# Kernel tuning notes

Measured on AMD Instinct MI355X. Metric: run time of the kernel, lower is better.

## Reference

```python
import jax, jax.numpy as jnp
import numpy as np

STEPS_PER_DAY = 144
HEADS = 4
MODEL_D = 152  # 24 input + 24 tod + 24 dow + 80 adaptive
HEAD_D = MODEL_D // HEADS
FF_D = 256
L = 12
PRED = 12
N = 358
B = 16
EVT_D = 1024
HID_EVT = 256
NUM_EVT = 4096
KMAX = 8
NEG = -1e30


def _layer_norm(x, g, b, eps=1e-5):
    m = jnp.mean(x, -1, keepdims=True)
    v = jnp.mean((x - m) ** 2, -1, keepdims=True)
    return (x - m) * jax.lax.rsqrt(v + eps) * g + b


def _mha(x, Wq, bq, Wk, bk, Wv, bv, Wo, bo):
    # x: (B, A, S, D); self-attention over axis S
    b_, a_, s_, d_ = x.shape
    q = (x @ Wq + bq).reshape(b_, a_, s_, HEADS, HEAD_D)
    k = (x @ Wk + bk).reshape(b_, a_, s_, HEADS, HEAD_D)
    v = (x @ Wv + bv).reshape(b_, a_, s_, HEADS, HEAD_D)
    scores = jnp.einsum('baqhd,bakhd->bahqk', q, k) * (HEAD_D ** -0.5)
    attn = jax.nn.softmax(scores, axis=-1)
    out = jnp.einsum('bahqk,bakhd->baqhd', attn, v).reshape(b_, a_, s_, d_)
    return out @ Wo + bo


def setup_inputs() -> dict:
    key = jax.random.key(0)
    ks = jax.random.split(key, 24)
    f32 = jnp.float32

    def nrm(k, shape, s=0.02):
        return jax.random.normal(k, shape, dtype=f32) * s

    inp = {}
    inp['var_x'] = jax.random.normal(ks[0], (B, L, N, 1), dtype=f32)
    inp['marker_x'] = jax.random.uniform(ks[1], (B, L, N, 4), dtype=f32)
    inp['W_in'] = nrm(ks[2], (3, 24)); inp['b_in'] = jnp.zeros((24,), f32)
    inp['tod_emb'] = nrm(ks[3], (STEPS_PER_DAY, 24))
    inp['dow_emb'] = nrm(ks[4], (7, 24))
    inp['adaptive_emb'] = nrm(ks[5], (L, N, 80))
    inp['Wq'] = nrm(ks[6], (6, MODEL_D, MODEL_D)); inp['bq'] = jnp.zeros((6, MODEL_D), f32)
    inp['Wk'] = nrm(ks[7], (6, MODEL_D, MODEL_D)); inp['bk'] = jnp.zeros((6, MODEL_D), f32)
    inp['Wv'] = nrm(ks[8], (6, MODEL_D, MODEL_D)); inp['bv'] = jnp.zeros((6, MODEL_D), f32)
    inp['Wo'] = nrm(ks[9], (6, MODEL_D, MODEL_D)); inp['bo'] = jnp.zeros((6, MODEL_D), f32)
    inp['W1'] = nrm(ks[10], (6, MODEL_D, FF_D)); inp['b1'] = jnp.zeros((6, FF_D), f32)
    inp['W2'] = nrm(ks[11], (6, FF_D, MODEL_D)); inp['b2'] = jnp.zeros((6, MODEL_D), f32)
    inp['ln1_g'] = jnp.ones((6, MODEL_D), f32); inp['ln1_b'] = jnp.zeros((6, MODEL_D), f32)
    inp['ln2_g'] = jnp.ones((6, MODEL_D), f32); inp['ln2_b'] = jnp.zeros((6, MODEL_D), f32)
    inp['event_embeddings'] = nrm(ks[12], (NUM_EVT + 1, EVT_D)).at[0].set(0.0)
    inp['W_evt'] = nrm(ks[13], (EVT_D, HID_EVT)); inp['b_evt'] = jnp.zeros((HID_EVT,), f32)
    inp['W_mm'] = nrm(ks[14], (L * (MODEL_D + HID_EVT), PRED)); inp['b_mm'] = jnp.zeros((PRED,), f32)
    inp['W_ts'] = nrm(ks[15], (L * MODEL_D, PRED)); inp['b_ts'] = jnp.zeros((PRED,), f32)
    inp['doy_indices'] = jax.random.randint(ks[16], (366, KMAX), 1, NUM_EVT + 1, dtype=jnp.int32)
    mask = jax.random.uniform(ks[17], (366, KMAX)) < 0.6
    inp['doy_mask'] = mask.at[:, 0].set(True)
    return inp


def reference(var_x, marker_x, W_in, b_in, tod_emb, dow_emb, adaptive_emb,
              Wq, bq, Wk, bk, Wv, bv, Wo, bo, W1, b1, W2, b2,
              ln1_g, ln1_b, ln2_g, ln2_b, event_embeddings, W_evt, b_evt,
              W_mm, b_mm, W_ts, b_ts, doy_indices, doy_mask):
    b_, l_, n_, _ = var_x.shape
    tod = jnp.clip((marker_x[..., 0] * STEPS_PER_DAY).astype(jnp.int32), 0, STEPS_PER_DAY - 1)
    dow = jnp.clip((marker_x[..., 1] * 7).astype(jnp.int32), 0, 6)
    x_in = jnp.concatenate([var_x, marker_x[..., 0:1], marker_x[..., 1:2]], axis=-1)
    x = jnp.concatenate([
        x_in @ W_in + b_in,
        tod_emb[tod],
        dow_emb[dow],
        jnp.broadcast_to(adaptive_emb[None], (b_, l_, n_, adaptive_emb.shape[-1])),
    ], axis=-1)  # (B, L, N, MODEL_D)
    # 3 temporal attention layers (over L), then 3 spatial (over N)
    for i in range(6):
        temporal = i < 3
        h = jnp.swapaxes(x, 1, 2) if temporal else x
        out = _mha(h, Wq[i], bq[i], Wk[i], bk[i], Wv[i], bv[i], Wo[i], bo[i])
        h = _layer_norm(h + out, ln1_g[i], ln1_b[i])
        ff = jax.nn.relu(h @ W1[i] + b1[i]) @ W2[i] + b2[i]
        h = _layer_norm(h + ff, ln2_g[i], ln2_b[i])
        x = jnp.swapaxes(h, 1, 2) if temporal else h
    ts_emb = jnp.swapaxes(x, 1, 2)  # (B, N, L, D)
    # ragged event gather + linear + masked max-pool (one vectorized pass)
    doy = jnp.clip((marker_x[:, -1, 0, 3] * 365).astype(jnp.int32), 0, 365)
    idx = doy_indices[doy]           # (B, KMAX)
    msk = doy_mask[doy]              # (B, KMAX)
    h_evt = event_embeddings[idx] @ W_evt + b_evt  # (B, KMAX, HID_EVT)
    evt = jnp.max(jnp.where(msk[..., None], h_evt, NEG), axis=1)  # (B, HID_EVT)
    evt_b = jnp.broadcast_to(evt[:, None, None, :], (b_, n_, l_, HID_EVT))
    fused = jnp.concatenate([evt_b, ts_emb], axis=-1).reshape(b_, n_, -1)
    mm_pred = fused @ W_mm + b_mm
    ts_pred = ts_emb.reshape(b_, n_, -1) @ W_ts + b_ts
    return jnp.swapaxes(mm_pred + ts_pred, 1, 2)  # (B, PRED, N)
```

## Files before the change

kernel.cpp:

```cpp
#include <hip/hip_runtime.h>
#include <hip/hip_bf16.h>

using bf = __hip_bfloat16;

#define B_   16
#define L_   12
#define N_   358
#define D_   152
#define TOK_ (B_*L_*N_)
#define FF_  256
#define HD_  38
#define SCALE_ 0.16222142113076254f
#define C2_   0.23403921469340696f

__device__ __forceinline__ float bf2f(bf x) { return __bfloat162float(x); }
__device__ __forceinline__ bf f2bf(float f) { return __float2bfloat16(f); }
__device__ __forceinline__ float lo_bf(unsigned u) { return __uint_as_float(u << 16); }
__device__ __forceinline__ float hi_bf(unsigned u) { return __uint_as_float(u & 0xffff0000u); }
__device__ __forceinline__ unsigned pk_bf(float a, float b) {
  union { bf h; unsigned short u; } A, Bu;
  A.h = f2bf(a); Bu.h = f2bf(b);
  return ((unsigned)Bu.u << 16) | A.u;
}
__device__ __forceinline__ ushort f2bf_u(float f) {
  union { bf h; ushort u; } t; t.h = f2bf(f); return t.u;
}

using short8  = __attribute__((ext_vector_type(8))) short;
using float4v = __attribute__((ext_vector_type(4))) float;

__device__ __forceinline__ void gl_lds16(const void* g, void* l) {
  __builtin_amdgcn_global_load_lds(
      (const __attribute__((address_space(1))) void*)g,
      (__attribute__((address_space(3))) void*)l, 16, 0, 0);
}

template<int SUBCB>
__device__ __forceinline__ void issue_w8(const char* gsrc, ushort* lds, int w, int lane) {
  constexpr int TB = SUBCB >> 10;
  constexpr int TAIL = SUBCB & 1023;
#pragma unroll
  for (int blk0 = 0; blk0 < TB; blk0 += 8) {
    int blk = blk0 + w;
    if (blk < TB)
      gl_lds16(gsrc + blk*1024 + (size_t)lane*16, (char*)lds + blk*1024);
  }
  if (TAIL) {
    if (w == (TB & 7) && lane < TAIL/16)
      gl_lds16(gsrc + TB*1024 + (size_t)lane*16, (char*)lds + TB*1024);
  }
}

template<int SUBCB>
__device__ __forceinline__ int issue_cnt(int w) {
  constexpr int TB = SUBCB >> 10;
  constexpr int TAIL = SUBCB & 1023;
  int n = (TB > 8 && w < TB - 8) ? 2 : 1;
  if (TAIL && w == (TB & 7)) n += 1;
  return n;
}

__device__ __forceinline__ void vm_wait(int n) {
  if (n == 1)      asm volatile("s_waitcnt vmcnt(1)" ::: "memory");
  else if (n == 2) asm volatile("s_waitcnt vmcnt(2)" ::: "memory");
  else             asm volatile("s_waitcnt vmcnt(3)" ::: "memory");
}

__device__ __forceinline__ short8 ld_g8(const ushort* p) {
  union { unsigned u[4]; short8 v; } t;
  t.u[0] = *(const unsigned*)(p);
  t.u[1] = *(const unsigned*)(p + 2);
  t.u[2] = *(const unsigned*)(p + 4);
  t.u[3] = *(const unsigned*)(p + 6);
  return t.v;
}

__global__ void k_beacon(float* out, int n, float val) {
  int i = blockIdx.x * 256 + threadIdx.x;
  if (i < n) out[i] = val;
}

#define WPREP_B 2700
#define EMB_B   269
#define EVT_B   128
#define WC_B    86
#define PREP_B  (WPREP_B + EMB_B + EVT_B + WC_B)

__device__ void d_wprep(int bid, int tid,
    const float* __restrict__ Wq, const float* __restrict__ Wk,
    const float* __restrict__ Wv, const float* __restrict__ Wo,
    const float* __restrict__ W1, const float* __restrict__ W2,
    unsigned* __restrict__ out) {
  int i = bid * 256 + tid;
  if (i >= 6*115200) return;
  int layer = i / 115200, r = i % 115200;
  const float* src; int K, Nd, d, up, c;
  if (r < 48000) {
    c = r / 9600; int rr = r % 9600; int m = rr / 3200; int r2 = rr % 3200;
    d = r2 / 20; up = r2 % 20;
    src = (m == 0 ? Wq : (m == 1 ? Wk : Wv)) + layer*23104; K = 152; Nd = 152;
  } else if (r < 64000) {
    int rr = r - 48000; c = rr / 3200; int r2 = rr % 3200;
    d = r2 / 20; up = r2 % 20;
    src = Wo + layer*23104; K = 152; Nd = 152;
  } else if (r < 89600) {
    int rr = r - 64000; c = rr / 5120; int r2 = rr % 5120;
    d = r2 / 20; up = r2 % 20;
    src = W1 + layer*38912; K = 152; Nd = 256;
  } else {
    int rr = r - 89600; c = rr / 3200; int r2 = rr % 3200;
    d = r2 / 20; up = r2 % 20;
    src = W2 + layer*38912; K = 256; Nd = 152;
  }
  float v0 = 0.f, v1 = 0.f;
  int k0 = 32*c + 2*up;
  if (up < 16 && d < Nd) {
    if (k0 < K)     v0 = src[(long)k0*Nd + d];
    if (k0 + 1 < K) v1 = src[(long)(k0+1)*Nd + d];
  }
  out[i] = pk_bf(v0, v1);
}

__device__ void d_embed(int bid, int tid,
    const float* __restrict__ var_x, const float* __restrict__ marker,
    const float* __restrict__ W_in, const float* __restrict__ b_in,
    const float* __restrict__ tod_emb, const float* __restrict__ dow_emb,
    const float* __restrict__ adap, bf* __restrict__ x) {
  int t = bid * 256 + tid;
  if (t >= TOK_) return;
  int n = t % N_;
  int l = (t / N_) % L_;
  float var = var_x[t];
  float m0 = marker[t*4 + 0];
  float m1 = marker[t*4 + 1];
  int tod = (int)(m0 * 144.f); tod = tod < 0 ? 0 : (tod > 143 ? 143 : tod);
  int dw  = (int)(m1 * 7.f);   dw  = dw  < 0 ? 0 : (dw  > 6   ? 6   : dw);
  bf* xp = x + (long)t * D_;
  for (int d = 0; d < 24; ++d)
    xp[d] = f2bf(var * W_in[d] + m0 * W_in[24 + d] + m1 * W_in[48 + d] + b_in[d]);
  for (int d = 0; d < 24; ++d) xp[24 + d] = f2bf(tod_emb[tod*24 + d]);
  for (int d = 0; d < 24; ++d) xp[48 + d] = f2bf(dow_emb[dw*24 + d]);
  for (int d = 0; d < 80; ++d) xp[72 + d] = f2bf(adap[(l*N_ + n)*80 + d]);
}

__device__ void d_evt1(int bk, int tid,
    const float* __restrict__ marker, const int* __restrict__ doy_idx,
    const float* __restrict__ emb, const float* __restrict__ W_evt,
    const float* __restrict__ b_evt, float* __restrict__ evt_h) {
  int b = bk >> 3; int ks = bk & 7;
  float m3 = marker[((b*L_ + (L_-1))*N_ + 0)*4 + 3];
  int doy = (int)(m3 * 365.f); doy = doy < 0 ? 0 : (doy > 365 ? 365 : doy);
  int idx = doy_idx[doy*8 + ks];
  if (idx < 0 || idx > 4096) idx = 0;
  int d = tid;
  float acc = b_evt[d];
  const float* er = emb + (long)idx * 1024;
  for (int e = 0; e < 1024; ++e)
    acc += er[e] * W_evt[e*256 + d];
  evt_h[bk*256 + d] = acc;
}

__device__ void d_wcomb(int bid, int tid,
    const float* __restrict__ W_mm, const float* __restrict__ W_ts,
    float* __restrict__ wcomb, float* __restrict__ wevtsum) {
  int i = bid * 256 + tid;
  if (i < 1824*12) {
    int r = i / 12, p = i % 12, l = r / 152, d = r % 152;
    wcomb[i] = W_mm[(l*408 + 256 + d)*12 + p] + W_ts[i];
  }
  if (i < 256*12) {
    int e = i / 12, p = i % 12;
    float s = 0.f;
    for (int l = 0; l < 12; ++l) s += W_mm[(l*408 + e)*12 + p];
    wevtsum[i] = s;
  }
}

__global__ __launch_bounds__(256) void k_prep(
    const float* Wq, const float* Wk, const float* Wv, const float* Wo,
    const float* W1, const float* W2, unsigned* wout,
    const float* var_x, const float* marker, const float* W_in,
    const float* b_in, const float* tod_emb, const float* dow_emb,
    const float* adap, bf* x,
    const int* doyi, const float* emb, const float* W_evt,
    const float* b_evt, float* evt_h,
    const float* W_mm, const float* W_ts, float* wcomb, float* wevtsum) {
  int bid = blockIdx.x, tid = threadIdx.x;
  if (bid < WPREP_B)
    d_wprep(bid, tid, Wq, Wk, Wv, Wo, W1, W2, wout);
  else if (bid < WPREP_B + EMB_B)
    d_embed(bid - WPREP_B, tid, var_x, marker, W_in, b_in, tod_emb, dow_emb, adap, x);
  else if (bid < WPREP_B + EMB_B + EVT_B)
    d_evt1(bid - WPREP_B - EMB_B, tid, marker, doyi, emb, W_evt, b_evt, evt_h);
  else
    d_wcomb(bid - WPREP_B - EMB_B - EVT_B, tid, W_mm, W_ts, wcomb, wevtsum);
}

template<int K, int Nd, int NW, int TOKB, int CSPLIT, bool RELU, bool LN>
__global__ __launch_bounds__(512) void k_gemm7(
    const bf* __restrict__ X, const ushort* __restrict__ Wg,
    const float* __restrict__ bi0, const float* __restrict__ bi1,
    const float* __restrict__ bi2, const bf* __restrict__ Res,
    const float* __restrict__ g, const float* __restrict__ bb,
    bf* __restrict__ Y0, bf* __restrict__ Y1, bf* __restrict__ Y2) {
  constexpr int NJ   = (Nd + 15) / 16;
  constexpr int NdP  = NJ * 16;
  constexpr int KC   = (K + 31) / 32;
  constexpr int G    = NW * CSPLIT;
  constexpr int S    = KC * G;
  constexpr int IR   = NdP / CSPLIT;
  constexpr int SUB_USH = IR * 40;
  constexpr int SUBCB   = SUB_USH * 2;
  constexpr int NJW  = IR / 32;
  constexpr int MR   = TOKB / 64;
  constexpr bool GLX = (K == 152);
  constexpr int XSTR = GLX ? K : (K + 8);
  __shared__ __align__(16) ushort Xs[TOKB * XSTR + 8];
  __shared__ __align__(16) ushort Wb[2 * SUB_USH];
  long row0 = (long)blockIdx.x * TOKB;
  int tid = threadIdx.x;
  int lane = tid & 63, w = tid >> 6;
  int cl = lane & 15, gr = lane >> 4;
  int wr = w >> 1, wc = w & 1;
  if constexpr (GLX) {
    constexpr int TBX = TOKB * K * 2 / 1024;
    const char* Xgc = (const char*)(X + row0 * K);
#pragma unroll
    for (int b0 = 0; b0 < TBX; b0 += 8) {
      int blk = b0 + w;
      if (blk < TBX)
        gl_lds16(Xgc + blk*1024 + (size_t)lane*16, (char*)Xs + blk*1024);
    }
  } else {
    const char* Xgc = (const char*)(X + row0 * K);
    for (int i = tid; i < TOKB*(K/8); i += 512) {
      int r = i / (K/8), c = i % (K/8);
      *(short8*)&Xs[r*XSTR + 8*c] = *(const short8*)(Xgc + r*(K*2) + c*16);
    }
    __syncthreads();
  }
  const char* gW = (const char*)Wg;
  issue_w8<SUBCB>(gW, Wb, w, lane);
  const int nw = issue_cnt<SUBCB>(w);
  float4v acc[G][MR][NJW];
#pragma unroll
  for (int gi = 0; gi < G; ++gi)
#pragma unroll
    for (int mi = 0; mi < MR; ++mi)
#pragma unroll
      for (int j = 0; j < NJW; ++j) acc[gi][mi][j] = (float4v){0.f,0.f,0.f,0.f};
#pragma unroll
  for (int s = 0; s < S; ++s) {
    if (s + 1 < S) {
      issue_w8<SUBCB>(gW + (size_t)(s+1)*SUBCB, Wb + ((s+1)&1)*SUB_USH, w, lane);
      vm_wait(nw);
    } else {
      asm volatile("s_waitcnt vmcnt(0)" ::: "memory");
    }
    __builtin_amdgcn_s_barrier();
    int kc = (s / G) * 32;
    const ushort* wb = Wb + (s&1)*SUB_USH;
    short8 af[MR];
#pragma unroll
    for (int mi = 0; mi < MR; ++mi)
      af[mi] = *(const short8*)&Xs[((TOKB/4)*wr + 16*mi + cl)*XSTR + kc + 8*gr];
#pragma unroll
    for (int j = 0; j < NJW; ++j) {
      short8 bv = *(const short8*)&wb[((IR/2)*wc + 16*j + cl)*40 + 8*gr];
#pragma unroll
      for (int mi = 0; mi < MR; ++mi)
        acc[s % G][mi][j] =
            __builtin_amdgcn_mfma_f32_16x16x32_bf16(af[mi], bv, acc[s % G][mi][j], 0, 0, 0);
    }
    asm volatile("s_waitcnt lgkmcnt(0)" ::: "memory");
    __builtin_amdgcn_s_barrier();
  }
  if constexpr (!LN) {
#pragma unroll
    for (int gi = 0; gi < G; ++gi) {
      bf* Y = (NW > 1) ? (gi == 0 ? Y0 : (gi == 1 ? Y1 : Y2)) : Y0;
      const float* bp = (NW > 1) ? (gi == 0 ? bi0 : (gi == 1 ? bi1 : bi2)) : bi0;
      int colb = (CSPLIT > 1 ? IR*gi : 0) + (IR/2)*wc;
#pragma unroll
      for (int j = 0; j < NJW; ++j) {
        int col = colb + 16*j + cl;
        if (col < Nd) {
          float bvs = bp[col];
#pragma unroll
          for (int mi = 0; mi < MR; ++mi) {
            long rw = row0 + (TOKB/4)*wr + 16*mi + 4*gr;
#pragma unroll
            for (int r = 0; r < 4; ++r) {
              float val = acc[gi][mi][j][r] + bvs;
              if (RELU) val = fmaxf(val, 0.f);
              Y[(rw + r) * Nd + col] = f2bf(val);
            }
          }
        }
      }
    }
  } else {
    float* LNb = (float*)Wb;
    int colb = (IR/2)*wc;
#pragma unroll
    for (int j = 0; j < NJW; ++j) {
      int col = colb + 16*j + cl;
      if (col < Nd) {
        float bvs = bi0[col];
#pragma unroll
        for (int mi = 0; mi < MR; ++mi) {
          long rw = row0 + (TOKB/4)*wr + 16*mi + 4*gr;
#pragma unroll
          for (int r = 0; r < 4; ++r)
            acc[0][mi][j][r] += bvs + bf2f(Res[(rw + r) * Nd + col]);
        }
      }
    }
    float mean[MR][4], rs[MR][4];
#pragma unroll
    for (int mi = 0; mi < MR; ++mi)
#pragma unroll
      for (int r = 0; r < 4; ++r) {
        float s = 0.f;
#pragma unroll
        for (int j = 0; j < NJW; ++j) s += acc[0][mi][j][r];
        s += __shfl_xor(s, 1, 64); s += __shfl_xor(s, 2, 64);
        s += __shfl_xor(s, 4, 64); s += __shfl_xor(s, 8, 64);
        if (cl == 0) LNb[((wr*MR + mi)*2 + wc)*16 + 4*gr + r] = s;
      }
    __syncthreads();
#pragma unroll
    for (int mi = 0; mi < MR; ++mi)
#pragma unroll
      for (int r = 0; r < 4; ++r) {
        float tot = LNb[((wr*MR + mi)*2 + 0)*16 + 4*gr + r]
                  + LNb[((wr*MR + mi)*2 + 1)*16 + 4*gr + r];
        mean[mi][r] = tot * (1.f / (float)Nd);
      }
#pragma unroll
    for (int mi = 0; mi < MR; ++mi)
#pragma unroll
      for (int r = 0; r < 4; ++r) {
        float s2 = 0.f;
#pragma unroll
        for (int j = 0; j < NJW; ++j) {
          int col = colb + 16*j + cl;
          if (col < Nd) {
            float dv = acc[0][mi][j][r] - mean[mi][r];
            s2 += dv*dv;
          }
        }
        s2 += __shfl_xor(s2, 1, 64); s2 += __shfl_xor(s2, 2, 64);
        s2 += __shfl_xor(s2, 4, 64); s2 += __shfl_xor(s2, 8, 64);
        if (cl == 0) LNb[256 + ((wr*MR + mi)*2 + wc)*16 + 4*gr + r] = s2;
      }
    __syncthreads();
#pragma unroll
    for (int mi = 0; mi < MR; ++mi)
#pragma unroll
      for (int r = 0; r < 4; ++r) {
        float tot2 = LNb[256 + ((wr*MR + mi)*2 + 0)*16 + 4*gr + r]
                   + LNb[256 + ((wr*MR + mi)*2 + 1)*16 + 4*gr + r];
        rs[mi][r] = rsqrtf(tot2 * (1.f / (float)Nd) + 1e-5f);
      }
#pragma unroll
    for (int j = 0; j < NJW; ++j) {
      int col = colb + 16*j + cl;
      if (col < Nd) {
        float gv = g[col], bv2 = bb[col];
#pragma unroll
        for (int mi = 0; mi < MR; ++mi) {
          long rw = row0 + (TOKB/4)*wr + 16*mi + 4*gr;
#pragma unroll
          for (int r = 0; r < 4; ++r)
            Y0[(rw + r) * Nd + col] =
                f2bf((acc[0][mi][j][r] - mean[mi][r]) * rs[mi][r] * gv + bv2);
        }
      }
    }
  }
}

__global__ __launch_bounds__(512) void k_ffn(
    const bf* __restrict__ X, const ushort* __restrict__ W1g,
    const ushort* __restrict__ W2g,
    const float* __restrict__ b1, const float* __restrict__ b2,
    const bf* __restrict__ Res, const float* __restrict__ g,
    const float* __restrict__ bb, bf* __restrict__ Y) {
  constexpr int S1 = 10, SUB1 = 5120;
  constexpr int S2 = 8,  SUB2 = 6400;
  constexpr int HSTR = 260;
  __shared__ __align__(16) ushort S_[29440];
  ushort* Xs  = S_;
  ushort* W1b = S_ + 9728;
  ushort* Hs  = S_;
  ushort* W2b = S_ + 16640;
  long row0 = (long)blockIdx.x * 64;
  int tid = threadIdx.x, lane = tid & 63, w = tid >> 6;
  int cl = lane & 15, gr = lane >> 4;
  int wr = w >> 1, wc = w & 1;
  {
    const char* Xgc = (const char*)(X + row0 * 152);
#pragma unroll
    for (int b0 = 0; b0 < 19; b0 += 8) {
      int blk = b0 + w;
      if (blk < 19)
        gl_lds16(Xgc + blk*1024 + (size_t)lane*16, (char*)Xs + blk*1024);
    }
  }
  issue_w8<SUB1*2>((const char*)W1g, W1b, w, lane);
  const int nw1 = issue_cnt<SUB1*2>(w);
  const int nw2 = issue_cnt<SUB2*2>(w);
  float4v acc1[2][4];
#pragma unroll
  for (int g2 = 0; g2 < 2; ++g2)
#pragma unroll
    for (int j = 0; j < 4; ++j) acc1[g2][j] = (float4v){0.f,0.f,0.f,0.f};
#pragma unroll
  for (int s = 0; s < S1; ++s) {
    if (s + 1 < S1) {
      issue_w8<SUB1*2>((const char*)W1g + (size_t)(s+1)*SUB1*2,
                       W1b + ((s+1)&1)*SUB1, w, lane);
      vm_wait(nw1);
    } else {
      asm volatile("s_waitcnt vmcnt(0)" ::: "memory");
    }
    __builtin_amdgcn_s_barrier();
    int kc = (s / 2) * 32;
    const ushort* wb = W1b + (s&1)*SUB1;
    short8 af = *(const short8*)&Xs[(16*wr + cl)*152 + kc + 8*gr];
#pragma unroll
    for (int j = 0; j < 4; ++j) {
      short8 bv = *(const short8*)&wb[(64*wc + 16*j + cl)*40 + 8*gr];
      acc1[s&1][j] =
          __builtin_amdgcn_mfma_f32_16x16x32_bf16(af, bv, acc1[s&1][j], 0, 0, 0);
    }
    asm volatile("s_waitcnt lgkmcnt(0)" ::: "memory");
    __builtin_amdgcn_s_barrier();
  }
#pragma unroll
  for (int g2 = 0; g2 < 2; ++g2)
#pragma unroll
    for (int j = 0; j < 4; ++j) {
      int col = g2*128 + 64*wc + 16*j + cl;
      float bvs = b1[col];
#pragma unroll
      for (int r = 0; r < 4; ++r) {
        int row = 16*wr + 4*gr + r;
        Hs[row*HSTR + col] = f2bf_u(fmaxf(acc1[g2][j][r] + bvs, 0.f));
      }
    }
  issue_w8<SUB2*2>((const char*)W2g, W2b, w, lane);
  asm volatile("s_waitcnt lgkmcnt(0)" ::: "memory");
  __builtin_amdgcn_s_barrier();
  float4v acc2[5];
#pragma unroll
  for (int j = 0; j < 5; ++j) acc2[j] = (float4v){0.f,0.f,0.f,0.f};
#pragma unroll
  for (int s = 0; s < S2; ++s) {
    if (s + 1 < S2) {
      issue_w8<SUB2*2>((const char*)W2g + (size_t)(s+1)*SUB2*2,
                       W2b + ((s+1)&1)*SUB2, w, lane);
      vm_wait(nw2);
    } else {
      asm volatile("s_waitcnt vmcnt(0)" ::: "memory");
    }
    __builtin_amdgcn_s_barrier();
    int kc = s * 32;
    const ushort* wb = W2b + (s&1)*SUB2;
    short8 af = *(const short8*)&Hs[(16*wr + cl)*HSTR + kc + 8*gr];
#pragma unroll
    for (int j = 0; j < 5; ++j) {
      short8 bv = *(const short8*)&wb[(80*wc + 16*j + cl)*40 + 8*gr];
      acc2[j] =
          __builtin_amdgcn_mfma_f32_16x16x32_bf16(af, bv, acc2[j], 0, 0, 0);
    }
    asm volatile("s_waitcnt lgkmcnt(0)" ::: "memory");
    __builtin_amdgcn_s_barrier();
  }
  float* LNb = (float*)W2b;
  int colb = 80*wc;
#pragma unroll
  for (int j = 0; j < 5; ++j) {
    int col = colb + 16*j + cl;
    if (col < D_) {
      float bvs = b2[col];
#pragma unroll
      for (int r = 0; r < 4; ++r)
        acc2[j][r] += bvs + bf2f(Res[(row0 + 16*wr + 4*gr + r) * D_ + col]);
    }
  }
  float mean[4], rsv[4];
#pragma unroll
  for (int r = 0; r < 4; ++r) {
    float s = 0.f;
#pragma unroll
    for (int j = 0; j < 5; ++j)
      if (colb + 16*j + cl < D_) s += acc2[j][r];
    s += __shfl_xor(s, 1, 64); s += __shfl_xor(s, 2, 64);
    s += __shfl_xor(s, 4, 64); s += __shfl_xor(s, 8, 64);
    if (cl == 0) LNb[(wr*2 + wc)*16 + 4*gr + r] = s;
  }
  __syncthreads();
#pragma unroll
  for (int r = 0; r < 4; ++r) {
    float tot = LNb[(wr*2 + 0)*16 + 4*gr + r] + LNb[(wr*2 + 1)*16 + 4*gr + r];
    mean[r] = tot * (1.f / (float)D_);
  }
#pragma unroll
  for (int r = 0; r < 4; ++r) {
    float s2 = 0.f;
#pragma unroll
    for (int j = 0; j < 5; ++j) {
      int col = colb + 16*j + cl;
      if (col < D_) { float dv = acc2[j][r] - mean[r]; s2 += dv*dv; }
    }
    s2 += __shfl_xor(s2, 1, 64); s2 += __shfl_xor(s2, 2, 64);
    s2 += __shfl_xor(s2, 4, 64); s2 += __shfl_xor(s2, 8, 64);
    if (cl == 0) LNb[128 + (wr*2 + wc)*16 + 4*gr + r] = s2;
  }
  __syncthreads();
#pragma unroll
  for (int r = 0; r < 4; ++r) {
    float tot2 = LNb[128 + (wr*2 + 0)*16 + 4*gr + r]
               + LNb[128 + (wr*2 + 1)*16 + 4*gr + r];
    rsv[r] = rsqrtf(tot2 * (1.f / (float)D_) + 1e-5f);
  }
#pragma unroll
  for (int j = 0; j < 5; ++j) {
    int col = colb + 16*j + cl;
    if (col < D_) {
      float gv = g[col], bv2 = bb[col];
#pragma unroll
      for (int r = 0; r < 4; ++r)
        Y[(row0 + 16*wr + 4*gr + r) * D_ + col] =
            f2bf((acc2[j][r] - mean[r]) * rsv[r] * gv + bv2);
    }
  }
}

__global__ __launch_bounds__(256) void k_attn_t2(
    const ushort* __restrict__ qg, const ushort* __restrict__ kg,
    const ushort* __restrict__ vg, bf* __restrict__ a) {
  int id = blockIdx.x; int b = id / N_; int n = id % N_;
  __shared__ ushort Ksh[4][16][40];
  __shared__ ushort Qsh[4][16][40];
  __shared__ ushort Vth[4][40][16];
  int tid = threadIdx.x;
  for (int i = tid; i < 1280; i += 256) {
    ((unsigned*)Ksh)[i] = 0u; ((unsigned*)Qsh)[i] = 0u; ((unsigned*)Vth)[i] = 0u;
  }
  __syncthreads();
  for (int i = tid; i < 4*12*19; i += 256) {
    int h = i / 228, r = i % 228, l = r / 19, t2 = r % 19;
    long off = ((long)(b*L_ + l) * N_ + n) * D_ + h*HD_ + 2*t2;
    *(unsigned*)&Ksh[h][l][2*t2] = *(const unsigned*)(kg + off);
    *(unsigned*)&Qsh[h][l][2*t2] = *(const unsigned*)(qg + off);
  }
  for (int i = tid; i < 4*12*19; i += 256) {
    int h = i / 228, r = i % 228, l = r / 19, t2 = r % 19;
    long off = ((long)(b*L_ + l) * N_ + n) * D_ + h*HD_ + 2*t2;
    unsigned u = *(const unsigned*)(vg + off);
    Vth[h][2*t2][l]     = (ushort)(u & 0xffffu);
    Vth[h][2*t2 + 1][l] = (ushort)(u >> 16);
  }
  __syncthreads();
  int lane = tid & 63, w = tid >> 6;
  int cl = lane & 15, gr = lane >> 4;
  const short8 z8 = {0,0,0,0,0,0,0,0};
  short8 a00 = *(const short8*)&Ksh[w][cl][8*gr];
  short8 qB0 = *(const short8*)&Qsh[w][cl][8*gr];
  short8 a01 = (gr == 0) ? *(const short8*)&Ksh[w][cl][32] : z8;
  short8 qB1 = (gr == 0) ? *(const short8*)&Qsh[w][cl][32] : z8;
  float4v sa = (float4v){0,0,0,0};
  sa = __builtin_amdgcn_mfma_f32_16x16x32_bf16(a00, qB0, sa, 0, 0, 0);
  sa = __builtin_amdgcn_mfma_f32_16x16x32_bf16(a01, qB1, sa, 0, 0, 0);
  float p[4];
#pragma unroll
  for (int r = 0; r < 4; ++r) {
    float xv = (4*gr + r < 12) ? sa[r]*C2_ : -1e30f;
    p[r] = __builtin_exp2f(fminf(xv, 80.f));
  }
  float sum_ = (p[0] + p[1]) + (p[2] + p[3]);
  sum_ += __shfl_xor(sum_, 16, 64);
  sum_ += __shfl_xor(sum_, 32, 64);
  unsigned u0 = pk_bf(p[0], p[1]);
  unsigned u1 = pk_bf(p[2], p[3]);
  int srcA = cl + 32*(gr & 1);
  int srcB = srcA + 16;
  unsigned w0 = __shfl(u0, srcA, 64), w1 = __shfl(u1, srcA, 64);
  unsigned w2 = __shfl(u0, srcB, 64), w3 = __shfl(u1, srcB, 64);
  union { unsigned u[4]; short8 v; } pbu;
  bool gv = gr < 2;
  pbu.u[0] = gv ? w0 : 0u; pbu.u[1] = gv ? w1 : 0u;
  pbu.u[2] = gv ? w2 : 0u; pbu.u[3] = gv ? w3 : 0u;
  short8 pB = pbu.v;
  float4v accO[3];
#pragma unroll
  for (int dt = 0; dt < 3; ++dt) {
    short8 aV = (gv && (dt < 2 || cl < 8))
        ? *(const short8*)&Vth[w][16*dt + cl][8*gr] : z8;
    accO[dt] = (float4v){0,0,0,0};
    accO[dt] = __builtin_amdgcn_mfma_f32_16x16x32_bf16(aV, pB, accO[dt], 0, 0, 0);
  }
  if (cl < 12) {
    float inv = 1.f / sum_;
    bf* ap = a + ((long)(b*L_ + cl) * N_ + n) * D_ + w*HD_;
#pragma unroll
    for (int dt = 0; dt < 2; ++dt) {
      *(unsigned*)(ap + 16*dt + 4*gr)     = pk_bf(accO[dt][0]*inv, accO[dt][1]*inv);
      *(unsigned*)(ap + 16*dt + 4*gr + 2) = pk_bf(accO[dt][2]*inv, accO[dt][3]*inv);
    }
    if (gr == 0) {
      *(unsigned*)(ap + 32) = pk_bf(accO[2][0]*inv, accO[2][1]*inv);
      *(unsigned*)(ap + 34) = pk_bf(accO[2][2]*inv, accO[2][3]*inv);
    } else if (gr == 1) {
      *(unsigned*)(ap + 36) = pk_bf(accO[2][0]*inv, accO[2][1]*inv);
    }
  }
}

__global__ __launch_bounds__(512) void k_attn_s6(
    const ushort* __restrict__ qg, const ushort* __restrict__ kg,
    const ushort* __restrict__ vg, bf* __restrict__ a) {
  __shared__ ushort Ks[360][40];
  __shared__ ushort Vt[38][392];
  int tid = threadIdx.x;
  int lane = tid & 63, w = tid >> 6;
  int cl = lane & 15, gr = lane >> 4;
  bool g0 = (gr == 0);
  const short8 z8 = {0,0,0,0,0,0,0,0};

  int id = blockIdx.x;
  int h = id & 3; int s = id >> 2;
  int b = s / L_; int l = s % L_;
  long base = (long)(b*L_ + l) * N_;
  for (int i = tid; i < 360*20; i += 512) {
    int j = i / 20, t2 = i % 20;
    unsigned u = 0u;
    if (j < N_ && t2 < 19)
      u = *(const unsigned*)(kg + (base + j)*D_ + h*HD_ + 2*t2);
    *(unsigned*)&Ks[j][2*t2] = u;
  }
  for (int i = tid; i < N_*19; i += 512) {
    int j = i / 19, t2 = i % 19;
    unsigned u = *(const unsigned*)(vg + (base + j)*D_ + h*HD_ + 2*t2);
    Vt[2*t2][j]     = (ushort)(u & 0xffffu);
    Vt[2*t2 + 1][j] = (ushort)(u >> 16);
  }
  for (int i = tid; i < 38*26; i += 512)
    Vt[i / 26][N_ + i % 26] = 0;
  __syncthreads();

  for (int qt = w; qt < 23; qt += 8) {
    const ushort* qp = qg + (base + 16*qt + cl) * D_ + h*HD_;
    short8 qB0 = ld_g8(qp + 8*gr);
    short8 qB1 = ld_g8(qp + 32 + 8*gr);
    float sum_ = 0.f;
    float4v accO[3];
    accO[0] = (float4v){0,0,0,0};
    accO[1] = (float4v){0,0,0,0};
    accO[2] = (float4v){0,0,0,0};
#pragma unroll 1
    for (int pr = 0; pr < 11; ++pr) {
      int k0 = 32*pr;
      int kr0 = k0 + cl;
      int kr1 = k0 + 16 + cl;
      float4v s0a = (float4v){0,0,0,0}, s1a = (float4v){0,0,0,0};
      {
        short8 a00 = *(const short8*)&Ks[kr0][8*gr];
        short8 a10 = *(const short8*)&Ks[kr1][8*gr];
        __builtin_amdgcn_s_setprio(1);
        s0a = __builtin_amdgcn_mfma_f32_16x16x32_bf16(a00, qB0, s0a, 0, 0, 0);
        s1a = __builtin_amdgcn_mfma_f32_16x16x32_bf16(a10, qB0, s1a, 0, 0, 0);
        short8 a01 = g0 ? *(const short8*)&Ks[kr0][32] : z8;
        short8 a11 = g0 ? *(const short8*)&Ks[kr1][32] : z8;
        s0a = __builtin_amdgcn_mfma_f32_16x16x32_bf16(a01, qB1, s0a, 0, 0, 0);
        s1a = __builtin_amdgcn_mfma_f32_16x16x32_bf16(a11, qB1, s1a, 0, 0, 0);
        __builtin_amdgcn_s_setprio(0);
      }
      float p0[4], p1[4];
#pragma unroll
      for (int r = 0; r < 4; ++r) {
        p0[r] = __builtin_exp2f(fminf(s0a[r]*C2_, 80.f));
        p1[r] = __builtin_exp2f(fminf(s1a[r]*C2_, 80.f));
      }
      sum_ += (p0[0] + p0[1]) + (p0[2] + p0[3])
            + (p1[0] + p1[1]) + (p1[2] + p1[3]);
      unsigned u0 = pk_bf(p0[0], p0[1]);
      unsigned u1 = pk_bf(p0[2], p0[3]);
      unsigned u2 = pk_bf(p1[0], p1[1]);
      unsigned u3 = pk_bf(p1[2], p1[3]);
      int srcA = cl + 16*((2*gr) & 3);
      int srcB = srcA + 16;
      unsigned a0 = __shfl(u0, srcA, 64), b0 = __shfl(u1, srcA, 64);
      unsigned c0 = __shfl(u0, srcB, 64), d0 = __shfl(u1, srcB, 64);
      unsigned a2 = __shfl(u2, srcA, 64), b2 = __shfl(u3, srcA, 64);
      unsigned c2 = __shfl(u2, srcB, 64), d2 = __shfl(u3, srcB, 64);
      bool lo = gr < 2;
      union { unsigned u[4]; short8 v; } pbu;
      pbu.u[0] = lo ? a0 : a2;
      pbu.u[1] = lo ? b0 : b2;
      pbu.u[2] = lo ? c0 : c2;
      pbu.u[3] = lo ? d0 : d2;
      short8 pB = pbu.v;
      __builtin_amdgcn_s_setprio(1);
#pragma unroll
      for (int dt = 0; dt < 3; ++dt) {
        short8 aV = (dt < 2 || cl < 6)
            ? *(const short8*)&Vt[16*dt + cl][k0 + 8*gr] : z8;
        accO[dt] = __builtin_amdgcn_mfma_f32_16x16x32_bf16(aV, pB, accO[dt], 0, 0, 0);
      }
      __builtin_amdgcn_s_setprio(0);
    }
    {
      int k0 = 352;
      int kr0 = k0 + cl; if (kr0 > 359) kr0 = 359;
      float4v s0a = (float4v){0,0,0,0};
      {
        short8 a00 = *(const short8*)&Ks[kr0][8*gr];
        s0a = __builtin_amdgcn_mfma_f32_16x16x32_bf16(a00, qB0, s0a, 0, 0, 0);
        short8 a01 = g0 ? *(const short8*)&Ks[kr0][32] : z8;
        s0a = __builtin_amdgcn_mfma_f32_16x16x32_bf16(a01, qB1, s0a, 0, 0, 0);
      }
      float p0[4];
#pragma unroll
      for (int r = 0; r < 4; ++r) {
        float xv = (4*gr + r < 6) ? s0a[r]*C2_ : -1e30f;
        p0[r] = __builtin_exp2f(fminf(xv, 80.f));
      }
      sum_ += (p0[0] + p0[1]) + (p0[2] + p0[3]);
      unsigned u0 = pk_bf(p0[0], p0[1]);
      unsigned u1 = pk_bf(p0[2], p0[3]);
      int srcA = cl + 16*((2*gr) & 3);
      int srcB = srcA + 16;
      unsigned a0 = __shfl(u0, srcA, 64), b0 = __shfl(u1, srcA, 64);
      unsigned c0 = __shfl(u0, srcB, 64), d0 = __shfl(u1, srcB, 64);
      bool lo = gr < 2;
      union { unsigned u[4]; short8 v; } pbu;
      pbu.u[0] = lo ? a0 : 0u;
      pbu.u[1] = lo ? b0 : 0u;
      pbu.u[2] = lo ? c0 : 0u;
      pbu.u[3] = lo ? d0 : 0u;
      short8 pB = pbu.v;
#pragma unroll
      for (int dt = 0; dt < 3; ++dt) {
        short8 aV = (dt < 2 || cl < 6)
            ? *(const short8*)&Vt[16*dt + cl][k0 + 8*gr] : z8;
        accO[dt] = __builtin_amdgcn_mfma_f32_16x16x32_bf16(aV, pB, accO[dt], 0, 0, 0);
      }
    }
    sum_ += __shfl_xor(sum_, 16, 64);
    sum_ += __shfl_xor(sum_, 32, 64);
    int qi = 16*qt + cl;
    if (qi < N_) {
      float inv = 1.f / sum_;
      bf* ap = a + (base + qi)*D_ + h*HD_;
#pragma unroll
      for (int dt = 0; dt < 2; ++dt) {
        *(unsigned*)(ap + 16*dt + 4*gr)     = pk_bf(accO[dt][0]*inv, accO[dt][1]*inv);
        *(unsigned*)(ap + 16*dt + 4*gr + 2) = pk_bf(accO[dt][2]*inv, accO[dt][3]*inv);
      }
      if (gr == 0) {
        *(unsigned*)(ap + 32) = pk_bf(accO[2][0]*inv, accO[2][1]*inv);
        *(unsigned*)(ap + 34) = pk_bf(accO[2][2]*inv, accO[2][3]*inv);
      } else if (gr == 1) {
        *(unsigned*)(ap + 36) = pk_bf(accO[2][0]*inv, accO[2][1]*inv);
      }
    }
  }
}

__global__ __launch_bounds__(256) void k_evtpool(
    const float* __restrict__ marker, const void* __restrict__ doy_mask,
    const float* __restrict__ evt_h, float* __restrict__ evtp) {
  __shared__ int hasF32, hasBig;
  if (threadIdx.x == 0) { hasF32 = 0; hasBig = 0; }
  __syncthreads();
  const unsigned* mw = (const unsigned*)doy_mask;
  for (int w = threadIdx.x; w < 732; w += 256) {
    unsigned u = mw[w];
    if (u == 0x3F800000u) hasF32 = 1;
    else if (u > 1u) hasBig = 1;
  }
  __syncthreads();
  int fmt = hasF32 ? 2 : (hasBig ? 1 : 0);
  int b = blockIdx.x;
  float m3 = marker[((b*L_ + (L_-1))*N_ + 0)*4 + 3];
  int doy = (int)(m3 * 365.f); doy = doy < 0 ? 0 : (doy > 365 ? 365 : doy);
  int j = threadIdx.x;
  float mx = -1e30f;
  for (int kx = 0; kx < 8; ++kx) {
    bool mk;
    if (fmt == 2)      mk = ((const float*)doy_mask)[doy*8 + kx] != 0.f;
    else if (fmt == 1) mk = ((const unsigned char*)doy_mask)[doy*8 + kx] != 0;
    else               mk = ((const int*)doy_mask)[doy*8 + kx] != 0;
    if (mk) mx = fmaxf(mx, evt_h[(b*8 + kx)*256 + j]);
  }
  evtp[b*256 + j] = mx;
}

__global__ __launch_bounds__(192) void k_final3(
    const bf* __restrict__ x, const float* __restrict__ wcomb,
    const float* __restrict__ wevtsum, const float* __restrict__ evtp,
    const float* __restrict__ b_mm, const float* __restrict__ b_ts,
    float* __restrict__ out) {
  int id = blockIdx.x; int b = id / N_; int n = id % N_;
  __shared__ float xs[1824];
  __shared__ float part[16][12];
  int tid = threadIdx.x;
  for (int e = tid; e < 912; e += 192) {
    int l = e / 76, du = e % 76;
    unsigned u = *(const unsigned*)((const ushort*)x +
        (((long)(b*L_ + l) * N_ + n) * 152 + 2*du));
    xs[l*152 + 2*du]     = lo_bf(u);
    xs[l*152 + 2*du + 1] = hi_bf(u);
  }
  __syncthreads();
  int g2 = tid / 12, p = tid % 12;
  float acc = 0.f;
  for (int e = g2; e < 1824; e += 16)
    acc += xs[e] * wcomb[e*12 + p];
  part[g2][p] = acc;
  __syncthreads();
  if (tid < 12) {
    float s = b_mm[tid] + b_ts[tid];
    for (int e = 0; e < 256; ++e) s += evtp[b*256 + e] * wevtsum[e*12 + tid];
    for (int gg = 0; gg < 16; ++gg) s += part[gg][tid];
    out[(b*12 + tid) * N_ + n] = s;
  }
}

extern "C" void kernel_launch(void* const* d_in, const int* in_sizes, int n_in,
                              void* d_out, int out_size, void* d_ws, size_t ws_size,
                              hipStream_t stream) {
  static const int expect[32] = {
    68736, 274944, 72, 24, 3456, 168, 343680,
    138624, 912, 138624, 912, 138624, 912, 138624, 912,
    233472, 1536, 233472, 912,
    912, 912, 912, 912,
    4195328, 262144, 256,
    58752, 12, 21888, 12,
    2928, 2928 };
  int nb = (out_size + 255)/256;
  if (n_in != 32) {
    k_beacon<<<nb, 256, 0, stream>>>((float*)d_out, out_size, 998.f);
    return;
  }
  for (int i = 0; i < 32; ++i) {
    if (in_sizes[i] != expect[i]) {
      k_beacon<<<nb, 256, 0, stream>>>((float*)d_out, out_size, 1000.f + i);
      return;
    }
  }
  if (out_size != 68736) {
    k_beacon<<<nb, 256, 0, stream>>>((float*)d_out, out_size, 997.f);
    return;
  }

  const float* var_x  = (const float*)d_in[0];
  const float* marker = (const float*)d_in[1];
  const float* W_in   = (const float*)d_in[2];
  const float* b_in   = (const float*)d_in[3];
  const float* tod    = (const float*)d_in[4];
  const float* dow    = (const float*)d_in[5];
  const float* adap   = (const float*)d_in[6];
  const float* Wq = (const float*)d_in[7];  const float* bq = (const float*)d_in[8];
  const float* Wk = (const float*)d_in[9];  const float* bk = (const float*)d_in[10];
  const float* Wv = (const float*)d_in[11]; const float* bv = (const float*)d_in[12];
  const float* Wo = (const float*)d_in[13]; const float* bo = (const float*)d_in[14];
  const float* W1 = (const float*)d_in[15]; const float* b1 = (const float*)d_in[16];
  const float* W2 = (const float*)d_in[17]; const float* b2 = (const float*)d_in[18];
  const float* g1 = (const float*)d_in[19]; const float* be1 = (const float*)d_in[20];
  const float* g2 = (const float*)d_in[21]; const float* be2 = (const float*)d_in[22];
  const float* emb   = (const float*)d_in[23];
  const float* W_evt = (const float*)d_in[24]; const float* b_evt = (const float*)d_in[25];
  const float* W_mm  = (const float*)d_in[26]; const float* b_mm  = (const float*)d_in[27];
  const float* W_ts  = (const float*)d_in[28]; const float* b_ts  = (const float*)d_in[29];
  const int* doyi = (const int*)d_in[30];
  const void* doym = d_in[31];

  const long TD = (long)TOK_ * D_;
  size_t need = (size_t)TD * 2 * 5
              + (size_t)(32768 + 4096 + 3072 + 21888) * 4
              + 2764800
              + 4096;
  if (ws_size < need) {
    k_beacon<<<nb, 256, 0, stream>>>((float*)d_out, out_size, (float)(ws_size >> 20));
    return;
  }

  bf* x = (bf*)d_ws;
  bf* q = x + TD;
  bf* k = q + TD;
  bf* v = k + TD;
  bf* a = v + TD;
  float* evt_h   = (float*)(a + TD);
  float* evtp    = evt_h + 32768;
  float* wevtsum = evtp + 4096;
  float* wcomb   = wevtsum + 3072;
  ushort* wprep  = (ushort*)(wcomb + 21888);

  k_prep<<<PREP_B, 256, 0, stream>>>(
      Wq, Wk, Wv, Wo, W1, W2, (unsigned*)wprep,
      var_x, marker, W_in, b_in, tod, dow, adap, x,
      doyi, emb, W_evt, b_evt, evt_h,
      W_mm, W_ts, wcomb, wevtsum);
  k_evtpool<<<16, 256, 0, stream>>>(marker, doym, evt_h, evtp);
  for (int i = 0; i < 6; ++i) {
    const ushort* pl = wprep + (size_t)i * 230400;
    k_gemm7<152,152,3,64,1,false,false><<<TOK_/64, 512, 0, stream>>>(
        x, pl, bq + i*152, bk + i*152, bv + i*152,
        nullptr, nullptr, nullptr, q, k, v);
    if (i < 3)
      k_attn_t2<<<B_*N_, 256, 0, stream>>>(
          (const ushort*)q, (const ushort*)k, (const ushort*)v, a);
    else
      k_attn_s6<<<B_*L_*4, 512, 0, stream>>>(
          (const ushort*)q, (const ushort*)k, (const ushort*)v, a);
    k_gemm7<152,152,1,128,1,false,true><<<TOK_/128, 512, 0, stream>>>(
        a, pl + 96000, bo + i*152, nullptr, nullptr,
        x, g1 + i*152, be1 + i*152, k, nullptr, nullptr);
    k_ffn<<<TOK_/64, 512, 0, stream>>>(
        k, pl + 128000, pl + 179200, b1 + i*256, b2 + i*152,
        k, g2 + i*152, be2 + i*152, x);
  }
  k_final3<<<B_*N_, 192, 0, stream>>>(x, wcomb, wevtsum, evtp, b_mm, b_ts,
                                      (float*)d_out);
}
```

Before: 1.077 ms.

## Fuse output projection, LayerNorm1 and FFN into a single per-layer kernel

Merges the Wo projection with residual add and first LayerNorm into the FFN kernel, so each 64-token block computes attention output projection, LN1, FFN and LN2 without writing the intermediate to global memory. The LN1 result is kept in LDS as the FFN input and in registers as the second residual, removing one kernel launch and a global write/read of the intermediate activations per layer. It also replaces the explicit vmcnt waits and split barriers with __syncthreads, which may weaken the load/compute overlap of the weight double buffering. The Wo GEMM now uses 64-row tiles instead of 128, and the output x is written in place while also being read as the residual, which is safe only because each block reads and writes the same rows.

Result: faster. 1.009 ms (median of 2 runs) (-6.3%).

```diff
diff --git a/kernel.cpp b/kernel.cpp
--- a/kernel.cpp
+++ b/kernel.cpp
@@ -381,36 +381,127 @@
   }
 }
 
-__global__ __launch_bounds__(512) void k_ffn(
-    const bf* __restrict__ X, const ushort* __restrict__ W1g,
+__global__ __launch_bounds__(512) void k_layer3(
+    const bf* __restrict__ A, const bf* __restrict__ Xres,
+    const ushort* __restrict__ Wog, const ushort* __restrict__ W1g,
     const ushort* __restrict__ W2g,
-    const float* __restrict__ b1, const float* __restrict__ b2,
-    const bf* __restrict__ Res, const float* __restrict__ g,
-    const float* __restrict__ bb, bf* __restrict__ Y) {
+    const float* __restrict__ bo, const float* __restrict__ b1,
+    const float* __restrict__ b2,
+    const float* __restrict__ g1v, const float* __restrict__ be1,
+    const float* __restrict__ g2v, const float* __restrict__ be2,
+    bf* __restrict__ Y) {
+  constexpr int S0 = 5,  SUB0 = 6400;
   constexpr int S1 = 10, SUB1 = 5120;
   constexpr int S2 = 8,  SUB2 = 6400;
   constexpr int HSTR = 260;
   __shared__ __align__(16) ushort S_[29440];
   ushort* Xs  = S_;
+  ushort* W0b = S_ + 9728;
   ushort* W1b = S_ + 9728;
-  ushort* Hs  = S_;
+  ushort* Hs2 = S_;
   ushort* W2b = S_ + 16640;
+  float*  LNb1 = (float*)(S_ + 22528);
   long row0 = (long)blockIdx.x * 64;
   int tid = threadIdx.x, lane = tid & 63, w = tid >> 6;
   int cl = lane & 15, gr = lane >> 4;
   int wr = w >> 1, wc = w & 1;
+  int colb = 80*wc;
   {
-    const char* Xgc = (const char*)(X + row0 * 152);
+    const char* Agc = (const char*)(A + row0 * 152);
 #pragma unroll
     for (int b0 = 0; b0 < 19; b0 += 8) {
       int blk = b0 + w;
       if (blk < 19)
-        gl_lds16(Xgc + blk*1024 + (size_t)lane*16, (char*)Xs + blk*1024);
+        gl_lds16(Agc + blk*1024 + (size_t)lane*16, (char*)Xs + blk*1024);
+    }
+  }
+  issue_w8<SUB0*2>((const char*)Wog, W0b, w, lane);
+  __syncthreads();
+  float4v acc0[5];
+#pragma unroll
+  for (int j = 0; j < 5; ++j) acc0[j] = (float4v){0.f,0.f,0.f,0.f};
+#pragma unroll
+  for (int s = 0; s < S0; ++s) {
+    if (s + 1 < S0)
+      issue_w8<SUB0*2>((const char*)Wog + (size_t)(s+1)*SUB0*2,
+                       W0b + ((s+1)&1)*SUB0, w, lane);
+    int kc = s * 32;
+    const ushort* wb = W0b + (s&1)*SUB0;
+    short8 af = *(const short8*)&Xs[(16*wr + cl)*152 + kc + 8*gr];
+#pragma unroll
+    for (int j = 0; j < 5; ++j) {
+      short8 bv = *(const short8*)&wb[(80*wc + 16*j + cl)*40 + 8*gr];
+      acc0[j] =
+          __builtin_amdgcn_mfma_f32_16x16x32_bf16(af, bv, acc0[j], 0, 0, 0);
+    }
+    __syncthreads();
+  }
+#pragma unroll
+  for (int j = 0; j < 5; ++j) {
+    int col = colb + 16*j + cl;
+    if (col < D_) {
+      float bvs = bo[col];
+#pragma unroll
+      for (int r = 0; r < 4; ++r)
+        acc0[j][r] += bvs + bf2f(Xres[(row0 + 16*wr + 4*gr + r) * D_ + col]);
+    }
+  }
+  float mean1[4], rsv1[4];
+#pragma unroll
+  for (int r = 0; r < 4; ++r) {
+    float s = 0.f;
+#pragma unroll
+    for (int j = 0; j < 5; ++j)
+      if (colb + 16*j + cl < D_) s += acc0[j][r];
+    s += __shfl_xor(s, 1, 64); s += __shfl_xor(s, 2, 64);
+    s += __shfl_xor(s, 4, 64); s += __shfl_xor(s, 8, 64);
+    if (cl == 0) LNb1[(wr*2 + wc)*16 + 4*gr + r] = s;
+  }
+  __syncthreads();
+#pragma unroll
+  for (int r = 0; r < 4; ++r) {
+    float tot = LNb1[(wr*2 + 0)*16 + 4*gr + r] + LNb1[(wr*2 + 1)*16 + 4*gr + r];
+    mean1[r] = tot * (1.f / (float)D_);
+  }
+#pragma unroll
+  for (int r = 0; r < 4; ++r) {
+    float s2 = 0.f;
+#pragma unroll
+    for (int j = 0; j < 5; ++j) {
+      int col = colb + 16*j + cl;
+      if (col < D_) { float dv = acc0[j][r] - mean1[r]; s2 += dv*dv; }
+    }
+    s2 += __shfl_xor(s2, 1, 64); s2 += __shfl_xor(s2, 2, 64);
+    s2 += __shfl_xor(s2, 4, 64); s2 += __shfl_xor(s2, 8, 64);
+    if (cl == 0) LNb1[128 + (wr*2 + wc)*16 + 4*gr + r] = s2;
+  }
+  __syncthreads();
+#pragma unroll
+  for (int r = 0; r < 4; ++r) {
+    float tot2 = LNb1[128 + (wr*2 + 0)*16 + 4*gr + r]
+               + LNb1[128 + (wr*2 + 1)*16 + 4*gr + r];
+    rsv1[r] = rsqrtf(tot2 * (1.f / (float)D_) + 1e-5f);
+  }
+  unsigned hres[5][2];
+#pragma unroll
+  for (int j = 0; j < 5; ++j) {
+    int col = colb + 16*j + cl;
+    if (col < D_) {
+      float gv = g1v[col], bv2 = be1[col];
+      ushort u[4];
+#pragma unroll
+      for (int r = 0; r < 4; ++r) {
+        u[r] = f2bf_u((acc0[j][r] - mean1[r]) * rsv1[r] * gv + bv2);
+        Xs[(16*wr + 4*gr + r)*152 + col] = u[r];
+      }
+      hres[j][0] = (unsigned)u[0] | ((unsigned)u[1] << 16);
+      hres[j][1] = (unsigned)u[2] | ((unsigned)u[3] << 16);
+    } else {
+      hres[j][0] = 0u; hres[j][1] = 0u;
     }
   }
   issue_w8<SUB1*2>((const char*)W1g, W1b, w, lane);
-  const int nw1 = issue_cnt<SUB1*2>(w);
-  const int nw2 = issue_cnt<SUB2*2>(w);
+  __syncthreads();
   float4v acc1[2][4];
 #pragma unroll
   for (int g2 = 0; g2 < 2; ++g2)
@@ -418,14 +509,9 @@
     for (int j = 0; j < 4; ++j) acc1[g2][j] = (float4v){0.f,0.f,0.f,0.f};
 #pragma unroll
   for (int s = 0; s < S1; ++s) {
-    if (s + 1 < S1) {
+    if (s + 1 < S1)
       issue_w8<SUB1*2>((const char*)W1g + (size_t)(s+1)*SUB1*2,
                        W1b + ((s+1)&1)*SUB1, w, lane);
-      vm_wait(nw1);
-    } else {
-      asm volatile("s_waitcnt vmcnt(0)" ::: "memory");
-    }
-    __builtin_amdgcn_s_barrier();
     int kc = (s / 2) * 32;
     const ushort* wb = W1b + (s&1)*SUB1;
     short8 af = *(const short8*)&Xs[(16*wr + cl)*152 + kc + 8*gr];
@@ -435,8 +521,7 @@
       acc1[s&1][j] =
           __builtin_amdgcn_mfma_f32_16x16x32_bf16(af, bv, acc1[s&1][j], 0, 0, 0);
     }
-    asm volatile("s_waitcnt lgkmcnt(0)" ::: "memory");
-    __builtin_amdgcn_s_barrier();
+    __syncthreads();
   }
 #pragma unroll
   for (int g2 = 0; g2 < 2; ++g2)
@@ -447,39 +532,31 @@
 #pragma unroll
       for (int r = 0; r < 4; ++r) {
         int row = 16*wr + 4*gr + r;
-        Hs[row*HSTR + col] = f2bf_u(fmaxf(acc1[g2][j][r] + bvs, 0.f));
+        Hs2[row*HSTR + col] = f2bf_u(fmaxf(acc1[g2][j][r] + bvs, 0.f));
       }
     }
   issue_w8<SUB2*2>((const char*)W2g, W2b, w, lane);
-  asm volatile("s_waitcnt lgkmcnt(0)" ::: "memory");
-  __builtin_amdgcn_s_barrier();
+  __syncthreads();
   float4v acc2[5];
 #pragma unroll
   for (int j = 0; j < 5; ++j) acc2[j] = (float4v){0.f,0.f,0.f,0.f};
 #pragma unroll
   for (int s = 0; s < S2; ++s) {
-    if (s + 1 < S2) {
+    if (s + 1 < S2)
       issue_w8<SUB2*2>((const char*)W2g + (size_t)(s+1)*SUB2*2,
                        W2b + ((s+1)&1)*SUB2, w, lane);
-      vm_wait(nw2);
-    } else {
-      asm volatile("s_waitcnt vmcnt(0)" ::: "memory");
-    }
-    __builtin_amdgcn_s_barrier();
     int kc = s * 32;
     const ushort* wb = W2b + (s&1)*SUB2;
-    short8 af = *(const short8*)&Hs[(16*wr + cl)*HSTR + kc + 8*gr];
+    short8 af = *(const short8*)&Hs2[(16*wr + cl)*HSTR + kc + 8*gr];
 #pragma unroll
     for (int j = 0; j < 5; ++j) {
       short8 bv = *(const short8*)&wb[(80*wc + 16*j + cl)*40 + 8*gr];
       acc2[j] =
           __builtin_amdgcn_mfma_f32_16x16x32_bf16(af, bv, acc2[j], 0, 0, 0);
     }
-    asm volatile("s_waitcnt lgkmcnt(0)" ::: "memory");
-    __builtin_amdgcn_s_barrier();
+    __syncthreads();
   }
   float* LNb = (float*)W2b;
-  int colb = 80*wc;
 #pragma unroll
   for (int j = 0; j < 5; ++j) {
     int col = colb + 16*j + cl;
@@ -487,7 +564,7 @@
       float bvs = b2[col];
 #pragma unroll
       for (int r = 0; r < 4; ++r)
-        acc2[j][r] += bvs + bf2f(Res[(row0 + 16*wr + 4*gr + r) * D_ + col]);
+        acc2[j][r] += bvs + ((r & 1) ? hi_bf(hres[j][r>>1]) : lo_bf(hres[j][r>>1]));
     }
   }
   float mean[4], rsv[4];
@@ -530,7 +607,7 @@
   for (int j = 0; j < 5; ++j) {
     int col = colb + 16*j + cl;
     if (col < D_) {
-      float gv = g[col], bv2 = bb[col];
+      float gv = g2v[col], bv2 = be2[col];
 #pragma unroll
       for (int r = 0; r < 4; ++r)
         Y[(row0 + 16*wr + 4*gr + r) * D_ + col] =
@@ -918,12 +995,10 @@
     else
       k_attn_s6<<<B_*L_*4, 512, 0, stream>>>(
           (const ushort*)q, (const ushort*)k, (const ushort*)v, a);
-    k_gemm7<152,152,1,128,1,false,true><<<TOK_/128, 512, 0, stream>>>(
-        a, pl + 96000, bo + i*152, nullptr, nullptr,
-        x, g1 + i*152, be1 + i*152, k, nullptr, nullptr);
-    k_ffn<<<TOK_/64, 512, 0, stream>>>(
-        k, pl + 128000, pl + 179200, b1 + i*256, b2 + i*152,
-        k, g2 + i*152, be2 + i*152, x);
+    k_layer3<<<TOK_/64, 512, 0, stream>>>(
+        a, x, pl + 96000, pl + 128000, pl + 179200,
+        bo + i*152, b1 + i*256, b2 + i*152,
+        g1 + i*152, be1 + i*152, g2 + i*152, be2 + i*152, x);
   }
   k_final3<<<B_*N_, 192, 0, stream>>>(x, wcomb, wevtsum, evtp, b_mm, b_ts,
                                       (float*)d_out);
```
